# Kernel optimization log

Measured on AMD Instinct MI355X. Metric: run time of the kernel, lower is better.

## Reference

```python
import jax, jax.numpy as jnp
import numpy as np

B, L, D = 8, 8192, 512   # batch, seq_len (q_len == kv_len), model dim
H, K = 8, 64             # heads, head_dim
W = 128                  # chunk width == stride (non-overlapping chunks)


def setup_inputs() -> dict:
    key = jax.random.key(0)
    ks = jax.random.split(key, 6)
    s = 1.0 / np.sqrt(D)
    return {
        "inputs_q": jax.random.normal(ks[0], (B, L, D), jnp.float32),
        "inputs_kv": jax.random.normal(ks[1], (B, L, D), jnp.float32),
        "Wq": jax.random.normal(ks[2], (D, H, K), jnp.float32) * s,
        "Wk": jax.random.normal(ks[3], (D, H, K), jnp.float32) * s,
        "Wv": jax.random.normal(ks[4], (D, H, K), jnp.float32) * s,
        "Wo": jax.random.normal(ks[5], (H, K, D), jnp.float32) * s,
    }


def reference(inputs_q, inputs_kv, Wq, Wk, Wv, Wo):
    # LocalAttentionLayer with q/kv_chunk_width == stride == W and
    # always_attend_to_first_position=True. Since width == stride the chunks
    # are non-overlapping, so the per-chunk Python loop of the original is
    # equivalent to a batched reshape into [B, C, W, ...] chunks. QKV
    # projections are position-wise, so projecting the full sequence first is
    # exactly the same math as projecting each chunk.
    C = L // W  # number of chunks
    scale = 1.0 / jnp.sqrt(jnp.asarray(K, inputs_q.dtype))

    q = jnp.einsum('bld,dhk->blhk', inputs_q, Wq) * scale  # [B,L,H,K]
    k = jnp.einsum('bld,dhk->blhk', inputs_kv, Wk)
    v = jnp.einsum('bld,dhk->blhk', inputs_kv, Wv)

    qc = q.reshape(B, C, W, H, K)
    kc = k.reshape(B, C, W, H, K)
    vc = v.reshape(B, C, W, H, K)

    # Global first KV position ([CLS]) prepended to every chunk's keys/values,
    # matching `kv_cls = inputs_kv[..., 0:1, :]; concat([kv_cls, chunk])`.
    k_cls = jnp.broadcast_to(k[:, None, 0:1], (B, C, 1, H, K))
    v_cls = jnp.broadcast_to(v[:, None, 0:1], (B, C, 1, H, K))
    kc = jnp.concatenate([k_cls, kc], axis=2)  # [B,C,W+1,H,K]
    vc = jnp.concatenate([v_cls, vc], axis=2)

    scores = jnp.einsum('bcqhk,bcmhk->bchqm', qc, kc)  # [B,C,H,W,W+1]
    attn = jax.nn.softmax(scores, axis=-1)
    ctx = jnp.einsum('bchqm,bcmhk->bcqhk', attn, vc)   # [B,C,W,H,K]
    ctx = ctx.reshape(B, L, H, K)
    return jnp.einsum('blhk,hkd->bld', ctx, Wo)        # [B,L,D]
```

## Files before the change

### kernel.cpp

```cpp
#include <hip/hip_runtime.h>
#include <hip/hip_bf16.h>
#include <type_traits>

#define B_ 8
#define L_ 8192
#define D_ 512
#define H_ 8
#define KD_ 64
#define W_ 128
#define C_ 64
#define M_ (B_ * L_)
#define HK_ 512

typedef __bf16 bf16_t;
typedef __bf16 bf16x8 __attribute__((ext_vector_type(8)));
typedef float f32x4 __attribute__((ext_vector_type(4)));

#define GLOAD16(gp, lp)                                                        \
  __builtin_amdgcn_global_load_lds(                                            \
      (const __attribute__((address_space(1))) unsigned int*)(gp),             \
      (__attribute__((address_space(3))) unsigned int*)(lp), 16, 0, 0)

#define WAIT_LGKM0()                                                           \
  do {                                                                         \
    asm volatile("s_waitcnt lgkmcnt(0)" ::: "memory");                         \
    __builtin_amdgcn_sched_barrier(0);                                         \
  } while (0)

#define MFMA16(AF, BF, ACC, OFF)                                               \
  do {                                                                         \
    __builtin_amdgcn_s_setprio(1);                                             \
    _Pragma("unroll") for (int i_ = 0; i_ < 4; i_++)                           \
        _Pragma("unroll") for (int j_ = 0; j_ < 4; j_++)                       \
            ACC[i_ + OFF][j_] = __builtin_amdgcn_mfma_f32_16x16x32_bf16(       \
                AF[i_], BF[j_], ACC[i_ + OFF][j_], 0, 0, 0);                   \
    __builtin_amdgcn_s_setprio(0);                                             \
  } while (0)

__global__ void prep_weights_kernel(const float* __restrict__ Wq,
                                    const float* __restrict__ Wk,
                                    const float* __restrict__ Wv,
                                    const float* __restrict__ Wo,
                                    bf16_t* __restrict__ wt) {
  const int n = blockIdx.x;
  const int mat = blockIdx.y;
  const float* src = (mat == 0) ? Wq : (mat == 1) ? Wk : (mat == 2) ? Wv : Wo;
  const float scale = (mat == 0) ? 0.125f : 1.0f;
  bf16_t* dst = wt + ((size_t)mat * 512 + n) * 512;
  for (int d = threadIdx.x; d < 512; d += blockDim.x) {
    dst[d] = (bf16_t)(src[(size_t)d * 512 + n] * scale);
  }
}

__device__ __forceinline__ bf16x8 rdfrag(const bf16_t* region, int rowbase,
                                         int lane) {
  const int fr = lane & 15;
  const int fs = (lane >> 4) ^ ((lane >> 1) & 3);
  return *reinterpret_cast<const bf16x8*>(region + (rowbase + fr) * 32 + fs * 8);
}

__device__ __forceinline__ void rdA_raw(const float* region, int rowbase,
                                        int lane, f32x4* o) {
  const int fr = lane & 15;
  const int g = lane >> 4;
  const int row = rowbase + fr;
  const int sw = row & 7;
  o[0] = *reinterpret_cast<const f32x4*>(region + row * 32 + (((g << 1)) ^ sw) * 4);
  o[1] = *reinterpret_cast<const f32x4*>(region + row * 32 + (((g << 1) | 1) ^ sw) * 4);
}

__device__ __forceinline__ bf16x8 cvtA(const f32x4* r) {
  bf16x8 o;
  o[0] = (bf16_t)r[0][0]; o[1] = (bf16_t)r[0][1];
  o[2] = (bf16_t)r[0][2]; o[3] = (bf16_t)r[0][3];
  o[4] = (bf16_t)r[1][0]; o[5] = (bf16_t)r[1][1];
  o[6] = (bf16_t)r[1][2]; o[7] = (bf16_t)r[1][3];
  return o;
}

template <int NTILE>
__global__ __launch_bounds__(512, 2)
void gemm_qkv(const float* __restrict__ A0f, const float* __restrict__ A1f,
              const bf16_t* __restrict__ BT,
              bf16_t* __restrict__ C0, bf16_t* __restrict__ C1,
              bf16_t* __restrict__ C2) {
  __shared__ __align__(16) bf16_t lds[65536];

  constexpr int NB = NTILE * 256;
  const int bid = blockIdx.x;
  const int swz = (bid & 7) * (NB / 8) + (bid >> 3);
  const int my = swz / NTILE;
  const int mx = swz - my * NTILE;
  const int m0 = my * 256;
  const int seg = mx >> 1;
  const int ncol0 = (mx & 1) * 256;
  const int nB0 = mx * 256;

  const float* const A = (seg == 0) ? A0f : A1f;
  bf16_t* const outp = (seg == 0) ? C0 : (seg == 1) ? C1 : C2;

  const int tid = threadIdx.x;
  const int lane = tid & 63;
  const int wid = tid >> 6;
  const int wmB = (wid >> 2) * 128;
  const int wnB = (wid & 3) * 64;

  const int sArow = lane >> 3;
  const int sAslot = (lane & 7) ^ sArow;
  const float* const Agb = A + ((size_t)m0 + wid * 8 + sArow) * 512 + sAslot * 4;
  const int sr0 = tid >> 2;
  const int sgs = (tid & 3) ^ ((sr0 >> 1) & 3);
  const bf16_t* const Bgb = BT + ((size_t)nB0 + sr0) * 512 + sgs * 8;

  auto astage = [&](int tile, int i) {
    char* lp = (char*)lds + (tile % 3) * 32768 + i * 8192 + wid * 1024;
    const float* g = Agb + (size_t)i * 64 * 512 + tile * 32;
    GLOAD16(g, lp);
  };
  auto bstage = [&](int tile) {
    char* lp = (char*)lds + 98304 + (tile & 1) * 16384 + wid * 1024;
    const bf16_t* g = Bgb + tile * 32;
    GLOAD16(g, lp);
    GLOAD16(g + (size_t)128 * 512, lp + 8192);
  };

  f32x4 acc[8][4] = {};
  bf16x8 b[4];

  astage(0, 0); astage(0, 1); astage(0, 2); astage(0, 3); bstage(0);
  astage(1, 0); astage(1, 1); astage(1, 2); astage(1, 3); bstage(1);
  asm volatile("s_waitcnt vmcnt(6)" ::: "memory");
  __builtin_amdgcn_s_barrier();

  for (int t = 0; t < 16; ++t) {
    const float* AR = (const float*)((char*)lds + (t % 3) * 32768);
    const bf16_t* BR = (const bf16_t*)((char*)lds + 98304 + (t & 1) * 16384);

    f32x4 ar0[4][2];
#pragma unroll
    for (int q = 0; q < 4; q++) rdA_raw(AR, wmB + q * 16, lane, ar0[q]);
#pragma unroll
    for (int q = 0; q < 4; q++) b[q] = rdfrag(BR, wnB + q * 16, lane);
    if (t < 14) { astage(t + 2, 0); astage(t + 2, 1); }
    __builtin_amdgcn_s_barrier();
    WAIT_LGKM0();
    {
      bf16x8 al[4];
#pragma unroll
      for (int q = 0; q < 4; q++) al[q] = cvtA(ar0[q]);
      MFMA16(al, b, acc, 0);
    }
    __builtin_amdgcn_s_barrier();

    f32x4 ar1[4][2];
#pragma unroll
    for (int q = 0; q < 4; q++) rdA_raw(AR, wmB + 64 + q * 16, lane, ar1[q]);
    if (t < 14) { astage(t + 2, 2); astage(t + 2, 3); bstage(t + 2); }
    __builtin_amdgcn_s_barrier();
    WAIT_LGKM0();
    {
      bf16x8 ah[4];
#pragma unroll
      for (int q = 0; q < 4; q++) ah[q] = cvtA(ar1[q]);
      MFMA16(ah, b, acc, 4);
    }
    if (t < 14) {
      asm volatile("s_waitcnt vmcnt(6)" ::: "memory");
    } else {
      asm volatile("s_waitcnt vmcnt(0)" ::: "memory");
    }
    __builtin_amdgcn_s_barrier();
  }

  const int crow = (lane >> 4) * 4;
  const int ccol = lane & 15;
#pragma unroll
  for (int i = 0; i < 8; i++) {
#pragma unroll
    for (int j = 0; j < 4; j++) {
      const int gm = m0 + wmB + i * 16 + crow;
      const int gn = ncol0 + wnB + j * 16 + ccol;
#pragma unroll
      for (int jj = 0; jj < 4; jj++)
        outp[(size_t)(gm + jj) * 512 + gn] = (bf16_t)acc[i][j][jj];
    }
  }
}

template <typename OT, int NTILE>
__global__ __launch_bounds__(512, 2)
void gemm256(const bf16_t* __restrict__ A0, const bf16_t* __restrict__ BT,
             OT* __restrict__ C0) {
  __shared__ __align__(16) bf16_t lds[65536];

  constexpr int NB = NTILE * 256;
  const int bid = blockIdx.x;
  const int swz = (bid & 7) * (NB / 8) + (bid >> 3);
  const int my = swz / NTILE;
  const int mx = swz - my * NTILE;
  const int m0 = my * 256;
  const int ncol0 = (mx & 1) * 256;
  const int nB0 = mx * 256;

  const int tid = threadIdx.x;
  const int lane = tid & 63;
  const int wid = tid >> 6;
  const int wmB = (wid >> 2) * 128;
  const int wnB = (wid & 3) * 64;

  const int sr0 = tid >> 2;
  const int sgs = (tid & 3) ^ ((sr0 >> 1) & 3);
  const bf16_t* const Agb = A0 + ((size_t)m0 + sr0) * 512 + sgs * 8;
  const bf16_t* const Bgb = BT + ((size_t)nB0 + sr0) * 512 + sgs * 8;

  auto stage = [&](int tile, int mat, int kh) {
    if (tile >= 8) return;
    bf16_t* reg = lds + ((tile & 1) * 4 + mat * 2 + kh) * 8192;
    const bf16_t* g0 = (mat == 0 ? Agb : Bgb) + tile * 64 + kh * 32;
    char* lp = (char*)reg + wid * 1024;
    GLOAD16(g0, lp);
    GLOAD16(g0 + (size_t)128 * 512, lp + 8192);
  };

  f32x4 acc[8][4] = {};
  bf16x8 a0[4], a1[4], a2[4], a3[4], b0[4], b2[4];

  stage(0, 0, 0); stage(0, 1, 0); stage(0, 0, 1); stage(0, 1, 1);
  stage(1, 1, 0); stage(1, 0, 0); stage(1, 1, 1);
  asm volatile("s_waitcnt vmcnt(6)" ::: "memory");
  __builtin_amdgcn_s_barrier();

  for (int t = 0; t < 8; ++t) {
    const int p = t & 1;
    const bf16_t* Ap0 = lds + (p * 4 + 0) * 8192;
    const bf16_t* Ap1 = lds + (p * 4 + 1) * 8192;
    const bf16_t* Bp0 = lds + (p * 4 + 2) * 8192;
    const bf16_t* Bp1 = lds + (p * 4 + 3) * 8192;

#pragma unroll
    for (int q = 0; q < 4; q++) a0[q] = rdfrag(Ap0, wmB + q * 16, lane);
#pragma unroll
    for (int q = 0; q < 4; q++) b0[q] = rdfrag(Bp0, wnB + q * 16, lane);
    stage(t + 1, 0, 1);
    __builtin_amdgcn_s_barrier();
    WAIT_LGKM0();
    if (t > 0) MFMA16(a3, b2, acc, 4);
    __builtin_amdgcn_s_barrier();

#pragma unroll
    for (int q = 0; q < 4; q++) a1[q] = rdfrag(Ap0, wmB + 64 + q * 16, lane);
    stage(t + 2, 1, 0);
    __builtin_amdgcn_s_barrier();
    WAIT_LGKM0();
    MFMA16(a0, b0, acc, 0);
    __builtin_amdgcn_s_barrier();

#pragma unroll
    for (int q = 0; q < 4; q++) a2[q] = rdfrag(Ap1, wmB + q * 16, lane);
#pragma unroll
    for (int q = 0; q < 4; q++) b2[q] = rdfrag(Bp1, wnB + q * 16, lane);
    stage(t + 2, 0, 0);
    __builtin_amdgcn_s_barrier();
    WAIT_LGKM0();
    MFMA16(a1, b0, acc, 4);
    __builtin_amdgcn_s_barrier();

#pragma unroll
    for (int q = 0; q < 4; q++) a3[q] = rdfrag(Ap1, wmB + 64 + q * 16, lane);
    stage(t + 2, 1, 1);
    __builtin_amdgcn_s_barrier();
    WAIT_LGKM0();
    MFMA16(a2, b2, acc, 0);
    if (t < 6) {
      asm volatile("s_waitcnt vmcnt(6)" ::: "memory");
    } else {
      asm volatile("s_waitcnt vmcnt(0)" ::: "memory");
    }
    __builtin_amdgcn_s_barrier();
  }

  MFMA16(a3, b2, acc, 4);

  const int crow = (lane >> 4) * 4;
  const int ccol = lane & 15;
#pragma unroll
  for (int i = 0; i < 8; i++) {
#pragma unroll
    for (int j = 0; j < 4; j++) {
      const int gm = m0 + wmB + i * 16 + crow;
      const int gn = ncol0 + wnB + j * 16 + ccol;
#pragma unroll
      for (int jj = 0; jj < 4; jj++) {
        const float vv = acc[i][j][jj];
        if constexpr (std::is_same<OT, float>::value)
          C0[(size_t)(gm + jj) * 512 + gn] = vv;
        else
          C0[(size_t)(gm + jj) * 512 + gn] = (bf16_t)vv;
      }
    }
  }
}

__global__ __launch_bounds__(256, 3)
void attn_kernel(const bf16_t* __restrict__ q, const bf16_t* __restrict__ k,
                 const bf16_t* __restrict__ v, bf16_t* __restrict__ ctx) {
  const int bid = blockIdx.x;
  const int swz = (bid & 7) * 512 + (bid >> 3);
  const int h = swz & 7;
  const int cb = swz >> 3;
  const int c = cb & 63;
  const int b = cb >> 6;

  const int tid = threadIdx.x;
  const int lane = tid & 63;
  const int w = tid >> 6;
  const int cl = lane & 15;
  const int g = lane >> 4;

  __shared__ bf16_t vT[64][136];
  __shared__ bf16_t pL[128][136];
  __shared__ float scl[128];
  __shared__ bf16_t kcls[64];
  __shared__ bf16_t vcls[64];

  const size_t headoff = (size_t)h * KD_;
  const size_t rowbase = (size_t)b * L_ + (size_t)c * W_;

  if (tid < 64) {
    kcls[tid] = k[(size_t)b * L_ * HK_ + headoff + tid];
    vcls[tid] = v[(size_t)b * L_ * HK_ + headoff + tid];
  }
  {
    const int m = tid >> 1;
    const int kd0 = (tid & 1) * 32;
    const bf16_t* vp = v + (rowbase + m) * HK_ + headoff + kd0;
#pragma unroll
    for (int i = 0; i < 4; i++) {
      bf16x8 t8 = *reinterpret_cast<const bf16x8*>(vp + i * 8);
#pragma unroll
      for (int j = 0; j < 8; j++) vT[kd0 + i * 8 + j][m] = t8[j];
    }
  }

  bf16x8 qf[2][2];
#pragma unroll
  for (int rt = 0; rt < 2; rt++)
#pragma unroll
    for (int kk = 0; kk < 2; kk++) {
      const size_t row = rowbase + w * 32 + rt * 16 + cl;
      qf[rt][kk] = *reinterpret_cast<const bf16x8*>(&q[row * HK_ + headoff + kk * 32 + g * 8]);
    }

  f32x4 sacc[2][8] = {};
#pragma unroll
  for (int ct = 0; ct < 8; ct++) {
    bf16x8 kf[2];
#pragma unroll
    for (int kk = 0; kk < 2; kk++) {
      const size_t rowm = rowbase + ct * 16 + cl;
      kf[kk] = *reinterpret_cast<const bf16x8*>(&k[rowm * HK_ + headoff + kk * 32 + g * 8]);
    }
#pragma unroll
    for (int rt = 0; rt < 2; rt++)
#pragma unroll
      for (int kk = 0; kk < 2; kk++)
        sacc[rt][ct] = __builtin_amdgcn_mfma_f32_16x16x32_bf16(qf[rt][kk], kf[kk], sacc[rt][ct], 0, 0, 0);
  }

  __syncthreads();

#pragma unroll
  for (int rt = 0; rt < 2; rt++) {
    float part = 0.f;
#pragma unroll
    for (int kk = 0; kk < 2; kk++)
#pragma unroll
      for (int j = 0; j < 8; j++)
        part += (float)qf[rt][kk][j] * (float)kcls[kk * 32 + g * 8 + j];
    part += __shfl_xor(part, 16);
    part += __shfl_xor(part, 32);
    if (g == 0) scl[w * 32 + rt * 16 + cl] = part;
  }

  float invd[2][4];
#pragma unroll
  for (int rt = 0; rt < 2; rt++) {
#pragma unroll
    for (int jj = 0; jj < 4; jj++) {
      float mx = sacc[rt][0][jj];
#pragma unroll
      for (int ct = 1; ct < 8; ct++) mx = fmaxf(mx, sacc[rt][ct][jj]);
#pragma unroll
      for (int d = 1; d < 16; d <<= 1) mx = fmaxf(mx, __shfl_xor(mx, d));
      const float sc = scl[w * 32 + rt * 16 + g * 4 + jj];
      mx = fmaxf(mx, sc);
      float sum = 0.f;
#pragma unroll
      for (int ct = 0; ct < 8; ct++) {
        const float e = __expf(sacc[rt][ct][jj] - mx);
        sacc[rt][ct][jj] = e;
        sum += e;
      }
#pragma unroll
      for (int d = 1; d < 16; d <<= 1) sum += __shfl_xor(sum, d);
      const float pc = __expf(sc - mx);
      sum += pc;
      const float inv = 1.0f / sum;
      invd[rt][jj] = inv;
      if (cl == 0) scl[w * 32 + rt * 16 + g * 4 + jj] = pc * inv;
    }
  }

#pragma unroll
  for (int rt = 0; rt < 2; rt++)
#pragma unroll
    for (int jj = 0; jj < 4; jj++) {
      const int row = w * 32 + rt * 16 + g * 4 + jj;
#pragma unroll
      for (int ct = 0; ct < 8; ct++)
        pL[row][ct * 16 + cl] = (bf16_t)(sacc[rt][ct][jj] * invd[rt][jj]);
    }
  __syncthreads();

  f32x4 cacc[2][4] = {};
#pragma unroll
  for (int kk = 0; kk < 4; kk++) {
    bf16x8 vf[4];
#pragma unroll
    for (int c2 = 0; c2 < 4; c2++)
      vf[c2] = *reinterpret_cast<const bf16x8*>(&vT[c2 * 16 + cl][kk * 32 + g * 8]);
#pragma unroll
    for (int rt = 0; rt < 2; rt++) {
      const bf16x8 pf = *reinterpret_cast<const bf16x8*>(&pL[w * 32 + rt * 16 + cl][kk * 32 + g * 8]);
#pragma unroll
      for (int c2 = 0; c2 < 4; c2++)
        cacc[rt][c2] = __builtin_amdgcn_mfma_f32_16x16x32_bf16(pf, vf[c2], cacc[rt][c2], 0, 0, 0);
    }
  }

#pragma unroll
  for (int rt = 0; rt < 2; rt++)
#pragma unroll
    for (int c2 = 0; c2 < 4; c2++)
#pragma unroll
      for (int jj = 0; jj < 4; jj++) {
        const int row = w * 32 + rt * 16 + g * 4 + jj;
        const int kd = c2 * 16 + cl;
        const float val = cacc[rt][c2][jj] + scl[row] * (float)vcls[kd];
        ctx[(rowbase + row) * HK_ + headoff + kd] = (bf16_t)val;
      }
}

extern "C" void kernel_launch(void* const* d_in, const int* in_sizes, int n_in,
                              void* d_out, int out_size, void* d_ws, size_t ws_size,
                              hipStream_t stream) {
  const float* Xq = (const float*)d_in[0];
  const float* Xkv = (const float*)d_in[1];
  const float* Wq = (const float*)d_in[2];
  const float* Wk = (const float*)d_in[3];
  const float* Wv = (const float*)d_in[4];
  const float* Wo = (const float*)d_in[5];
  float* out = (float*)d_out;

  char* ws = (char*)d_ws;
  bf16_t* wT = (bf16_t*)ws;
  size_t off = (size_t)4 * 512 * 512 * sizeof(bf16_t);
  bf16_t* qb = (bf16_t*)(ws + off); off += (size_t)M_ * HK_ * 2;
  bf16_t* kb = (bf16_t*)(ws + off); off += (size_t)M_ * HK_ * 2;
  bf16_t* vb = (bf16_t*)(ws + off); off += (size_t)M_ * HK_ * 2;
  bf16_t* ctxb = (bf16_t*)(ws + off);

  bf16_t* wTqkv = wT;
  bf16_t* wTo = wT + (size_t)3 * 512 * 512;

  prep_weights_kernel<<<dim3(512, 4), 128, 0, stream>>>(Wq, Wk, Wv, Wo, wT);

  gemm_qkv<6><<<dim3(6 * (M_ / 256)), 512, 0, stream>>>(
      Xq, Xkv, wTqkv, qb, kb, vb);

  attn_kernel<<<dim3(H_ * C_ * B_), 256, 0, stream>>>(qb, kb, vb, ctxb);

  gemm256<float, 2><<<dim3(2 * (M_ / 256)), 512, 0, stream>>>(ctxb, wTo, out);
}
```

Measured before the change: 354.5 us.

## Tile weight transpose via LDS and restructure fp32 A-tile staging layout

```diff
diff --git a/kernel.cpp b/kernel.cpp
--- a/kernel.cpp
+++ b/kernel.cpp
@@ -42,13 +42,23 @@
                                     const float* __restrict__ Wv,
                                     const float* __restrict__ Wo,
                                     bf16_t* __restrict__ wt) {
-  const int n = blockIdx.x;
-  const int mat = blockIdx.y;
+  __shared__ float t[64][65];
+  const int tid = threadIdx.x;
+  const int mat = blockIdx.z;
   const float* src = (mat == 0) ? Wq : (mat == 1) ? Wk : (mat == 2) ? Wv : Wo;
   const float scale = (mat == 0) ? 0.125f : 1.0f;
-  bf16_t* dst = wt + ((size_t)mat * 512 + n) * 512;
-  for (int d = threadIdx.x; d < 512; d += blockDim.x) {
-    dst[d] = (bf16_t)(src[(size_t)d * 512 + n] * scale);
+  const int d0 = blockIdx.x * 64, n0 = blockIdx.y * 64;
+  const int c = tid & 63, rb = tid >> 6;
+#pragma unroll
+  for (int i = 0; i < 16; i++) {
+    const int r = i * 4 + rb;
+    t[r][c] = src[(size_t)(d0 + r) * 512 + n0 + c];
+  }
+  __syncthreads();
+#pragma unroll
+  for (int i = 0; i < 16; i++) {
+    const int n = i * 4 + rb;
+    wt[((size_t)mat * 512 + n0 + n) * 512 + d0 + c] = (bf16_t)(t[c][n] * scale);
   }
 }
 
@@ -64,9 +74,11 @@
   const int fr = lane & 15;
   const int g = lane >> 4;
   const int row = rowbase + fr;
-  const int sw = row & 7;
-  o[0] = *reinterpret_cast<const f32x4*>(region + row * 32 + (((g << 1)) ^ sw) * 4);
-  o[1] = *reinterpret_cast<const f32x4*>(region + row * 32 + (((g << 1) | 1) ^ sw) * 4);
+  const int sw = (row >> 1) & 3;
+  const float* sub = region + (g >> 1) * 4096;
+  const int s0 = (g & 1) << 1;
+  o[0] = *reinterpret_cast<const f32x4*>(sub + row * 16 + ((s0 | 0) ^ sw) * 4);
+  o[1] = *reinterpret_cast<const f32x4*>(sub + row * 16 + ((s0 | 1) ^ sw) * 4);
 }
 
 __device__ __forceinline__ bf16x8 cvtA(const f32x4* r) {
@@ -105,16 +117,17 @@
   const int wmB = (wid >> 2) * 128;
   const int wnB = (wid & 3) * 64;
 
-  const int sArow = lane >> 3;
-  const int sAslot = (lane & 7) ^ sArow;
-  const float* const Agb = A + ((size_t)m0 + wid * 8 + sArow) * 512 + sAslot * 4;
+  const float* const Agb =
+      A + ((size_t)m0 + (tid >> 2)) * 512 + (((tid & 3) ^ ((tid >> 3) & 3))) * 4;
   const int sr0 = tid >> 2;
   const int sgs = (tid & 3) ^ ((sr0 >> 1) & 3);
   const bf16_t* const Bgb = BT + ((size_t)nB0 + sr0) * 512 + sgs * 8;
 
   auto astage = [&](int tile, int i) {
-    char* lp = (char*)lds + (tile % 3) * 32768 + i * 8192 + wid * 1024;
-    const float* g = Agb + (size_t)i * 64 * 512 + tile * 32;
+    const int sub = i >> 1, half = i & 1;
+    char* lp = (char*)lds + (tile % 3) * 32768 + sub * 16384 + half * 8192 +
+               wid * 1024;
+    const float* g = Agb + (size_t)half * 128 * 512 + tile * 32 + sub * 16;
     GLOAD16(g, lp);
   };
   auto bstage = [&](int tile) {
@@ -473,7 +486,7 @@
   bf16_t* wTqkv = wT;
   bf16_t* wTo = wT + (size_t)3 * 512 * 512;
 
-  prep_weights_kernel<<<dim3(512, 4), 128, 0, stream>>>(Wq, Wk, Wv, Wo, wT);
+  prep_weights_kernel<<<dim3(8, 8, 4), 256, 0, stream>>>(Wq, Wk, Wv, Wo, wT);
 
   gemm_qkv<6><<<dim3(6 * (M_ / 256)), 512, 0, stream>>>(
       Xq, Xkv, wTqkv, qb, kb, vb);
```

Result: no change. 356.8 us (+0.6%).
